# Performance work log

Measured on AMD Instinct MI355X. Metric: run time of the kernel, lower is better.

## Reference

```python
import jax, jax.numpy as jnp
import numpy as np

# dims
N, E, C, HH, HEADS, A, V, D, AE, FH, MAXEL = 10000, 80000, 64, 128, 8, 32, 16, 64, 32, 128, 100
L, K = 2, 9  # lmax=2 -> (L+1)^2 = 9 steerable coefficients
EXPAND = jnp.array([0, 1, 1, 1, 2, 2, 2, 2, 2])          # coeff -> degree l
EXP1 = jnp.array([0, 0, 0, 1, 1, 1, 1, 1])                # coeffs 1..8 -> l-1
L_ONEHOT = jax.nn.one_hot(EXPAND, 3, dtype=jnp.float32)   # [9,3]
COUNTS = jnp.array([1 * C, 3 * C, 5 * C], dtype=jnp.float32)


def so3_linear(h, W, b):
    # per-degree linear (SO3_LinearV2): W [3,Cin,Cout], bias only on l=0
    out = jnp.einsum('nkc,kcd->nkd', h, W[EXPAND])
    return out.at[:, 0].add(b)


def enorm(h):
    # equivariant norm: per-node, per-degree RMS over (m, channels)
    sq = jnp.einsum('nkc,kl->nl', h * h, L_ONEHOT)        # [N,3] sum of squares per l
    scale = jax.lax.rsqrt(sq / COUNTS + 1e-6)             # [N,3]
    return h * scale[:, EXPAND][:, :, None]


def seg_softmax(logits, seg, n):
    m = jax.ops.segment_max(logits, seg, num_segments=n)
    m = jnp.where(jnp.isfinite(m), m, 0.0)
    e = jnp.exp(logits - m[seg])
    s = jax.ops.segment_sum(e, seg, num_segments=n)
    return e / (s[seg] + 1e-9)


def smooth_leaky_relu(z, a=0.2):
    return a * z + (1.0 - a) * z * jax.nn.sigmoid(z)


def setup_inputs():
    key = jax.random.key(0)
    ks = jax.random.split(key, 20)
    p = lambda i, sh, s=0.05: jax.random.normal(ks[i], sh, jnp.float32) * s
    return {
        'x': jax.random.normal(ks[0], (N, K, C), jnp.float32),
        'edge_distance': jax.random.uniform(ks[1], (E, D), dtype=jnp.float32),
        'rl_ij': jax.random.normal(ks[2], (E, K - 1), jnp.float32),
        'src_emb': p(3, (MAXEL, AE), 0.001),
        'tgt_emb': p(4, (MAXEL, AE), 0.001),
        'W1': p(5, (D + 2 * AE, 128)), 'b1': jnp.zeros((128,), jnp.float32),
        'W2': p(6, (128, 3 * 2 * C)), 'b2': jnp.zeros((3 * 2 * C,), jnp.float32),
        'W_conv1': p(7, (3, 2 * C, HH)),
        'W_m0': p(8, (2 * C, HEADS * A + HH + 2 * L * HH)),
        'ln_g': jnp.ones((A,), jnp.float32), 'ln_b': jnp.zeros((A,), jnp.float32),
        'alpha_dot': p(9, (HEADS, A), 0.2),
        'W_xj': p(10, (C, HH)),
        'W_conv2': p(11, (3, HH, HEADS * V)),
        'W_proj': p(12, (3, HEADS * V, C)), 'b_proj': jnp.zeros((C,), jnp.float32),
        'W_gate': p(13, (C, FH)), 'b_gate': jnp.zeros((FH,), jnp.float32),
        'W_ffn1': p(14, (3, C, FH)), 'b_ffn1': jnp.zeros((FH,), jnp.float32),
        'W_ffn2': p(15, (3, FH, C)), 'b_ffn2': jnp.zeros((C,), jnp.float32),
        'atomic_numbers': jax.random.randint(ks[16], (N,), 0, MAXEL),
        'edge_index': jax.random.randint(ks[17], (2, E), 0, N),
    }


def _block(x, edge_distance, rl_ij, src_emb, tgt_emb, W1, b1, W2, b2, W_conv1,
           W_m0, ln_g, ln_b, alpha_dot, W_xj, W_conv2, W_proj, b_proj,
           W_gate, b_gate, W_ffn1, b_ffn1, W_ffn2, b_ffn2,
           atomic_numbers, edge_index):
    src, tgt = edge_index[0], edge_index[1]
    # ---- attention branch (pre-norm) ----
    xn = enorm(x)
    xs, xt = xn[src], xn[tgt]                                    # [E,9,C] gathers
    x_edge = jnp.concatenate([xs, xt], axis=-1)                  # [E,9,2C]
    # radial function with source/target atom embeddings (use_m_share_rad)
    ef = jnp.concatenate([edge_distance, src_emb[atomic_numbers[src]],
                          tgt_emb[atomic_numbers[tgt]]], axis=-1)
    rad = jax.nn.silu(ef @ W1 + b1) @ W2 + b2                    # [E, 3*2C]
    rad = rad.reshape(E, 3, 2 * C)[:, EXPAND]                    # [E,9,2C]
    x_edge = x_edge * rad
    # so2_conv_1: per-degree linear + extra m0 scalar outputs
    msg = jnp.einsum('ekc,kcd->ekd', x_edge, W_conv1[EXPAND])    # [E,9,HH]
    extra = x_edge[:, 0] @ W_m0                                  # [E,896]
    alpha_f = extra[:, :HEADS * A].reshape(E, HEADS, A)
    g_scalar = extra[:, HEADS * A:HEADS * A + HH]                # [E,HH]
    gates = extra[:, HEADS * A + HH:].reshape(E, 2, L, HH)
    g_dir = jax.nn.sigmoid(gates[:, 0])[:, EXP1]                 # [E,8,HH]
    g_ten = jax.nn.sigmoid(gates[:, 1])[:, EXP1]                 # [E,8,HH]
    # GATA value activation: scalar silu + gated direction/tensor terms (l>=1)
    xj_proj = jnp.einsum('ekc,cd->ekd', xs, W_xj)                # [E,9,HH]
    val0 = jax.nn.silu(g_scalar)                                 # [E,HH]
    val_rest = msg[:, 1:] + rl_ij[:, :, None] * g_dir + xj_proj[:, 1:] * g_ten
    val = jnp.concatenate([val0[:, None], val_rest], axis=1)     # [E,9,HH]
    # so2_conv_2
    vout = jnp.einsum('ekd,kdh->ekh', val, W_conv2[EXPAND])      # [E,9,H*V]
    # attention weights
    mu = jnp.mean(alpha_f, axis=-1, keepdims=True)
    var = jnp.var(alpha_f, axis=-1, keepdims=True)
    an = (alpha_f - mu) * jax.lax.rsqrt(var + 1e-5) * ln_g + ln_b
    logits = jnp.einsum('eha,ha->eh', smooth_leaky_relu(an), alpha_dot)
    attn = seg_softmax(logits, tgt, N)                           # [E,HEADS]
    vout = vout.reshape(E, K, HEADS, V) * attn[:, None, :, None]
    node_out = jax.ops.segment_sum(vout.reshape(E, K, HEADS * V), tgt,
                                   num_segments=N)               # [N,9,H*V]
    x = x + so3_linear(node_out, W_proj, b_proj)
    # ---- FFN branch (pre-norm, separable S2-style gating) ----
    yn = enorm(x)
    g = yn[:, 0] @ W_gate + b_gate                               # [N,FH]
    h = so3_linear(yn, W_ffn1, b_ffn1)                           # [N,9,FH]
    h = jnp.concatenate([jax.nn.silu(g)[:, None],
                         h[:, 1:] * jax.nn.sigmoid(g)[:, None, :]], axis=1)
    return x + so3_linear(h, W_ffn2, b_ffn2)


def reference(x, edge_distance, rl_ij, src_emb, tgt_emb, W1, b1, W2, b2,
              W_conv1, W_m0, ln_g, ln_b, alpha_dot, W_xj, W_conv2, W_proj,
              b_proj, W_gate, b_gate, W_ffn1, b_ffn1, W_ffn2, b_ffn2,
              atomic_numbers, edge_index):
    return _block(x, edge_distance, rl_ij, src_emb, tgt_emb, W1, b1, W2, b2,
                  W_conv1, W_m0, ln_g, ln_b, alpha_dot, W_xj, W_conv2, W_proj,
                  b_proj, W_gate, b_gate, W_ffn1, b_ffn1, W_ffn2, b_ffn2,
                  atomic_numbers, edge_index)
```

## Files before the change

kernel.cpp:

```cpp
#include <hip/hip_runtime.h>

#define NN 10000
#define EE 80000

__device__ __forceinline__ float bf2f(unsigned short u) {
  return __uint_as_float(((unsigned)u) << 16);
}
__device__ __forceinline__ unsigned short f2bf(float f) {
  unsigned u = __float_as_uint(f);
  return (unsigned short)((u + 0x7FFFu + ((u >> 16) & 1u)) >> 16);
}
__device__ __forceinline__ float sigm(float x) { return 1.0f / (1.0f + __expf(-x)); }
__device__ __forceinline__ float siluf(float x) { return x * sigm(x); }

__device__ __forceinline__ float ld1(const void* p, long i, bool isf) {
  return isf ? ((const float*)p)[i] : bf2f(((const unsigned short*)p)[i]);
}
__device__ __forceinline__ void st1(void* p, long i, float v, bool isf) {
  if (isf) ((float*)p)[i] = v;
  else     ((unsigned short*)p)[i] = f2bf(v);
}
struct F8 { float v[8]; };
__device__ __forceinline__ F8 ld8(const void* p, long i, bool isf) {
  F8 r;
  if (isf) {
    const float* q = (const float*)p + i;
    float4 a = *(const float4*)q;
    float4 b = *(const float4*)(q + 4);
    r.v[0] = a.x; r.v[1] = a.y; r.v[2] = a.z; r.v[3] = a.w;
    r.v[4] = b.x; r.v[5] = b.y; r.v[6] = b.z; r.v[7] = b.w;
  } else {
    uint4 u = *(const uint4*)((const unsigned short*)p + i);
    r.v[0] = __uint_as_float(u.x << 16); r.v[1] = __uint_as_float(u.x & 0xFFFF0000u);
    r.v[2] = __uint_as_float(u.y << 16); r.v[3] = __uint_as_float(u.y & 0xFFFF0000u);
    r.v[4] = __uint_as_float(u.z << 16); r.v[5] = __uint_as_float(u.z & 0xFFFF0000u);
    r.v[6] = __uint_as_float(u.w << 16); r.v[7] = __uint_as_float(u.w & 0xFFFF0000u);
  }
  return r;
}
__device__ __forceinline__ void ld4v(const void* p, long i, bool isf, float o[4]) {
  if (isf) {
    float4 v = *(const float4*)((const float*)p + i);
    o[0] = v.x; o[1] = v.y; o[2] = v.z; o[3] = v.w;
  } else {
    uint2 u = *(const uint2*)((const unsigned short*)p + i);
    o[0] = bf2f((unsigned short)u.x); o[1] = bf2f((unsigned short)(u.x >> 16));
    o[2] = bf2f((unsigned short)u.y); o[3] = bf2f((unsigned short)(u.y >> 16));
  }
}
__device__ __forceinline__ void ldx4(const unsigned short* p, long i, float o[4]) {
  uint2 u = *(const uint2*)(p + i);
  o[0] = bf2f((unsigned short)u.x); o[1] = bf2f((unsigned short)(u.x >> 16));
  o[2] = bf2f((unsigned short)u.y); o[3] = bf2f((unsigned short)(u.y >> 16));
}
__device__ __forceinline__ void st4bf(unsigned short* dst, float a, float b,
                                      float c, float d) {
  uint2 u;
  u.x = (unsigned)f2bf(a) | ((unsigned)f2bf(b) << 16);
  u.y = (unsigned)f2bf(c) | ((unsigned)f2bf(d) << 16);
  *(uint2*)dst = u;
}
__device__ __forceinline__ float u8f(unsigned v) {
  return (float)(v & 0xFFu) * (1.f / 255.f);
}

typedef __attribute__((ext_vector_type(8))) short bf8v;
typedef __attribute__((ext_vector_type(4))) float f4v;
struct AF128 { bf8v a[4]; };
struct AF64  { bf8v a[2]; };
struct BF128 { bf8v b[4]; };
struct BF64  { bf8v b[2]; };

__device__ __forceinline__ AF128 load_af128(const unsigned short* sA, int pitch, int lane) {
  AF128 f;
  const unsigned short* p = sA + (lane & 15) * pitch + ((lane >> 4) << 3);
#pragma unroll
  for (int kb = 0; kb < 4; ++kb) f.a[kb] = *(const bf8v*)(p + kb * 32);
  return f;
}
__device__ __forceinline__ AF64 load_af64(const unsigned short* sA, int pitch, int lane) {
  AF64 f;
  const unsigned short* p = sA + (lane & 15) * pitch + ((lane >> 4) << 3);
#pragma unroll
  for (int kb = 0; kb < 2; ++kb) f.a[kb] = *(const bf8v*)(p + kb * 32);
  return f;
}
__device__ __forceinline__ BF128 load_b128(const unsigned short* Wt, int row0, int lane) {
  BF128 f;
  const unsigned short* p = Wt + (long)(row0 + (lane & 15)) * 128 + ((lane >> 4) << 3);
#pragma unroll
  for (int kb = 0; kb < 4; ++kb) f.b[kb] = *(const bf8v*)(p + kb * 32);
  return f;
}
__device__ __forceinline__ BF64 load_b64f(const unsigned short* Wt, int row0, int lane) {
  BF64 f;
  const unsigned short* p = Wt + (long)(row0 + (lane & 15)) * 64 + ((lane >> 4) << 3);
#pragma unroll
  for (int kb = 0; kb < 2; ++kb) f.b[kb] = *(const bf8v*)(p + kb * 32);
  return f;
}
__device__ __forceinline__ f4v mfma128f(const AF128& a, const BF128& w) {
  f4v acc = {0.f, 0.f, 0.f, 0.f};
#pragma unroll
  for (int kb = 0; kb < 4; ++kb)
    acc = __builtin_amdgcn_mfma_f32_16x16x32_bf16(a.a[kb], w.b[kb], acc, 0, 0, 0);
  return acc;
}
__device__ __forceinline__ f4v mfma64f(const AF64& a, const BF64& w) {
  f4v acc = {0.f, 0.f, 0.f, 0.f};
#pragma unroll
  for (int kb = 0; kb < 2; ++kb)
    acc = __builtin_amdgcn_mfma_f32_16x16x32_bf16(a.a[kb], w.b[kb], acc, 0, 0, 0);
  return acc;
}
__device__ __forceinline__ f4v mfma128w(const BF128& w, const AF128& x) {
  f4v acc = {0.f, 0.f, 0.f, 0.f};
#pragma unroll
  for (int kb = 0; kb < 4; ++kb)
    acc = __builtin_amdgcn_mfma_f32_16x16x32_bf16(w.b[kb], x.a[kb], acc, 0, 0, 0);
  return acc;
}
__device__ __forceinline__ f4v mfma64w(const BF64& w, const AF64& x) {
  f4v acc = {0.f, 0.f, 0.f, 0.f};
#pragma unroll
  for (int kb = 0; kb < 2; ++kb)
    acc = __builtin_amdgcn_mfma_f32_16x16x32_bf16(w.b[kb], x.a[kb], acc, 0, 0, 0);
  return acc;
}
__device__ __forceinline__ f4v mfma128(const AF128& f, const unsigned short* Wt,
                                       int row0, int lane) {
  return mfma128f(f, load_b128(Wt, row0, lane));
}
__device__ __forceinline__ f4v mfma64(const AF64& f, const unsigned short* Wt,
                                      int row0, int lane) {
  return mfma64f(f, load_b64f(Wt, row0, lane));
}
__device__ __forceinline__ void store8(unsigned short* dst, const unsigned short v[8]) {
  uint4 u;
  u.x = (unsigned)v[0] | ((unsigned)v[1] << 16);
  u.y = (unsigned)v[2] | ((unsigned)v[3] << 16);
  u.z = (unsigned)v[4] | ((unsigned)v[5] << 16);
  u.w = (unsigned)v[6] | ((unsigned)v[7] << 16);
  *(uint4*)dst = u;
}

#define OFF_W1 0
#define OFF_W2 16384
#define OFF_M0 65536
#define OFF_C1 180224
#define OFF_XJ 229376
#define OFF_C2 237568
#define OFF_PJ 286720
#define OFF_G  311296
#define OFF_F1 319488
#define OFF_F2 344064
#define WT_TOTAL 368640

#define WS_SBUF   1177280
#define WS_LOGB   1497280
#define WS_CURS   2777280
#define WS_PERM   2817280
#define WS_NOUT   3137280
#define WS_XN     49217280

__global__ __launch_bounds__(256) void k_repack(
    const void* __restrict__ W1, const void* __restrict__ W2,
    const void* __restrict__ W_m0, const void* __restrict__ W_conv1,
    const void* __restrict__ W_xj, const void* __restrict__ W_conv2,
    const void* __restrict__ W_proj, const void* __restrict__ W_gate,
    const void* __restrict__ W_ffn1, const void* __restrict__ W_ffn2,
    const void* __restrict__ ln_g, unsigned short* __restrict__ wt) {
  const bool isf = (((const unsigned*)ln_g)[0] == 0x3F800000u);
  int i = blockIdx.x * 256 + threadIdx.x;
  float v;
  if (i < 16384)       { int n = i >> 7, k = i & 127; v = ld1(W1, (long)k * 128 + n, isf); }
  else if (i < 65536)  { int j = i - 16384; int n = j >> 7, k = j & 127;
                         v = ld1(W2, (long)k * 384 + n, isf); }
  else if (i < 180224) { int j = i - 65536; int n = j >> 7, k = j & 127;
                         v = ld1(W_m0, (long)k * 896 + n, isf); }
  else if (i < 229376) { int j = i - 180224; int l = j >> 14, r = j & 16383;
                         int n = r >> 7, k = r & 127;
                         v = ld1(W_conv1, (long)(l * 128 + k) * 128 + n, isf); }
  else if (i < 237568) { int j = i - 229376; int n = j >> 6, k = j & 63;
                         v = ld1(W_xj, (long)k * 128 + n, isf); }
  else if (i < 286720) { int j = i - 237568; int l = j >> 14, r = j & 16383;
                         int n = r >> 7, k = r & 127;
                         v = ld1(W_conv2, (long)(l * 128 + k) * 128 + n, isf); }
  else if (i < 311296) { int j = i - 286720; int l = j >> 13, r = j & 8191;
                         int n = r >> 7, k = r & 127;
                         v = ld1(W_proj, (long)(l * 128 + k) * 64 + n, isf); }
  else if (i < 319488) { int j = i - 311296; int n = j >> 6, k = j & 63;
                         v = ld1(W_gate, (long)k * 128 + n, isf); }
  else if (i < 344064) { int j = i - 319488; int l = j >> 13, r = j & 8191;
                         int n = r >> 6, k = r & 63;
                         v = ld1(W_ffn1, (long)(l * 64 + k) * 128 + n, isf); }
  else                 { int j = i - 344064; int l = j >> 13, r = j & 8191;
                         int n = r >> 7, k = r & 127;
                         v = ld1(W_ffn2, (long)(l * 128 + k) * 64 + n, isf); }
  wt[i] = f2bf(v);
}

__global__ __launch_bounds__(256) void k_scales(const void* __restrict__ x,
                                                const void* __restrict__ ln_g,
                                                unsigned short* __restrict__ xn) {
  const bool isf = (((const unsigned*)ln_g)[0] == 0x3F800000u);
  const int n = blockIdx.x * 4 + (threadIdx.x >> 6);
  const int c = threadIdx.x & 63;
  long xb = (long)n * 576;
  float v[9];
#pragma unroll
  for (int k = 0; k < 9; ++k) v[k] = ld1(x, xb + k * 64 + c, isf);
  float q0 = v[0] * v[0], q1 = 0.f, q2 = 0.f;
#pragma unroll
  for (int k = 1; k < 4; ++k) q1 += v[k] * v[k];
#pragma unroll
  for (int k = 4; k < 9; ++k) q2 += v[k] * v[k];
#pragma unroll
  for (int off = 32; off > 0; off >>= 1) {
    q0 += __shfl_xor(q0, off); q1 += __shfl_xor(q1, off); q2 += __shfl_xor(q2, off);
  }
  float s0 = rsqrtf(q0 * (1.f / 64.f)  + 1e-6f);
  float s1 = rsqrtf(q1 * (1.f / 192.f) + 1e-6f);
  float s2 = rsqrtf(q2 * (1.f / 320.f) + 1e-6f);
  xn[xb + c] = f2bf(v[0] * s0);
#pragma unroll
  for (int k = 1; k < 4; ++k) xn[xb + k * 64 + c] = f2bf(v[k] * s1);
#pragma unroll
  for (int k = 4; k < 9; ++k) xn[xb + k * 64 + c] = f2bf(v[k] * s2);
}

__global__ void k_init0(float* __restrict__ p) {
  int i = blockIdx.x * 256 + threadIdx.x;
  if (i < 80000) p[i] = 0.f;
}
__global__ void k_initn(float4* __restrict__ p) {
  int i = blockIdx.x * 256 + threadIdx.x;
  p[i] = make_float4(0.f, 0.f, 0.f, 0.f);
}
__global__ void k_zc(int* __restrict__ c) {
  int i = blockIdx.x * 256 + threadIdx.x;
  if (i < NN) c[i] = 0;
}
__global__ void k_hist(const int* __restrict__ edge_index, int* __restrict__ cnt) {
  int e = blockIdx.x * 256 + threadIdx.x;
  if (e < EE) atomicAdd(&cnt[edge_index[EE + e]], 1);
}
__global__ __launch_bounds__(256) void k_prefix(int* __restrict__ cur) {
  __shared__ int part[256], off0[256];
  const int th = threadIdx.x;
  int cnt[40]; int s = 0;
#pragma unroll 1
  for (int i = 0; i < 40; ++i) {
    int n = th * 40 + i;
    cnt[i] = (n < NN) ? cur[n] : 0;
    s += cnt[i];
  }
  part[th] = s;
  __syncthreads();
  if (th == 0) {
    int acc = 0;
    for (int i = 0; i < 256; ++i) { off0[i] = acc; acc += part[i]; }
  }
  __syncthreads();
  int acc = off0[th];
#pragma unroll 1
  for (int i = 0; i < 40; ++i) {
    int n = th * 40 + i;
    if (n < NN) { cur[n] = acc; acc += cnt[i]; }
  }
}
__global__ void k_scatter(const int* __restrict__ edge_index, int* __restrict__ cur,
                          int* __restrict__ perm) {
  int e = blockIdx.x * 256 + threadIdx.x;
  if (e < EE) {
    int tg = edge_index[EE + e];
    int pos = atomicAdd(&cur[tg], 1);
    perm[pos] = e;
  }
}

__global__ __launch_bounds__(256) void k_logits_e(
    const unsigned short* __restrict__ xn, const void* __restrict__ dist,
    const void* __restrict__ src_emb, const void* __restrict__ tgt_emb,
    const void* __restrict__ b1, const void* __restrict__ b2,
    const void* __restrict__ ln_g, const void* __restrict__ ln_b,
    const void* __restrict__ alpha_dot,
    const int* __restrict__ an, const int* __restrict__ edge_index,
    const unsigned short* __restrict__ wt,
    unsigned short* __restrict__ logitsb, float* __restrict__ sbuf) {
  const bool isf = (((const unsigned*)ln_g)[0] == 0x3F800000u);
  __shared__ int s_src[32], s_tgt[32], s_as[32], s_at[32];
  __shared__ __align__(16) unsigned short sA[32 * 136];
  __shared__ __align__(16) unsigned short sA2[32 * 136];
  __shared__ __align__(16) unsigned short sFB[32 * 264];

  const int t = threadIdx.x;
  const int e0 = blockIdx.x * 32;
  const int lane = t & 63, wave = t >> 6, lm = lane & 15, lq = lane >> 4;

  if (t < 32) {
    int eid = e0 + t;
    int s = edge_index[eid], g = edge_index[EE + eid];
    s_src[t] = s; s_tgt[t] = g;
    s_as[t] = an[s]; s_at[t] = an[g];
  }
  __syncthreads();
#pragma unroll
  for (int ee = 0; ee < 2; ++ee) {
    int e = ee * 16 + (t >> 4), c0 = (t & 15) * 8;
    int eid = e0 + e;
    F8 vv;
    if (c0 < 64)      vv = ld8(dist, (long)eid * 64 + c0, isf);
    else if (c0 < 96) vv = ld8(src_emb, (long)s_as[e] * 32 + (c0 - 64), isf);
    else              vv = ld8(tgt_emb, (long)s_at[e] * 32 + (c0 - 96), isf);
    unsigned short v8[8];
#pragma unroll
    for (int j = 0; j < 8; ++j) v8[j] = f2bf(vv.v[j]);
    store8(&sA[e * 136 + c0], v8);
  }
  __syncthreads();
  {
    AF128 fa0 = load_af128(sA, 136, lane);
    AF128 fa1 = load_af128(sA + 16 * 136, 136, lane);
#pragma unroll
    for (int i = 0; i < 2; ++i) {
      int nt = wave + 4 * i;
      BF128 w = load_b128(wt + OFF_W1, nt * 16, lane);
      f4v d0 = mfma128w(w, fa0);
      f4v d1 = mfma128w(w, fa1);
      int hc = nt * 16 + lq * 4;
      float bb[4]; ld4v(b1, hc, isf, bb);
      st4bf(&sA2[lm * 136 + hc],
            siluf(d0[0] + bb[0]), siluf(d0[1] + bb[1]),
            siluf(d0[2] + bb[2]), siluf(d0[3] + bb[3]));
      st4bf(&sA2[(16 + lm) * 136 + hc],
            siluf(d1[0] + bb[0]), siluf(d1[1] + bb[1]),
            siluf(d1[2] + bb[2]), siluf(d1[3] + bb[3]));
    }
  }
  __syncthreads();
  {
    AF128 fh0 = load_af128(sA2, 136, lane);
    AF128 fh1 = load_af128(sA2 + 16 * 136, 136, lane);
#pragma unroll
    for (int i = 0; i < 2; ++i) {
      int nt = wave + 4 * i;
      BF128 w = load_b128(wt + OFF_W2, nt * 16, lane);
      f4v dd[2] = { mfma128w(w, fh0), mfma128w(w, fh1) };
      int rc = nt * 16 + lq * 4;
      float bb[4]; ld4v(b2, rc, isf, bb);
#pragma unroll
      for (int g = 0; g < 2; ++g) {
        int m = g * 16 + lm;
        float xv[4];
        if (rc < 64) ldx4(xn, (long)s_src[m] * 576 + rc, xv);
        else         ldx4(xn, (long)s_tgt[m] * 576 + (rc - 64), xv);
        st4bf(&sA[m * 136 + rc],
              (dd[g][0] + bb[0]) * xv[0], (dd[g][1] + bb[1]) * xv[1],
              (dd[g][2] + bb[2]) * xv[2], (dd[g][3] + bb[3]) * xv[3]);
      }
    }
  }
  __syncthreads();
  {
    AF128 fe0 = load_af128(sA, 136, lane);
    AF128 fe1 = load_af128(sA + 16 * 136, 136, lane);
#pragma unroll
    for (int i = 0; i < 4; ++i) {
      int nt = wave + 4 * i;
      BF128 w = load_b128(wt + OFF_M0, nt * 16, lane);
      f4v d0 = mfma128w(w, fe0);
      f4v d1 = mfma128w(w, fe1);
      int ac = nt * 16 + lq * 4;
      st4bf(&sFB[lm * 264 + ac], d0[0], d0[1], d0[2], d0[3]);
      st4bf(&sFB[(16 + lm) * 264 + ac], d1[0], d1[1], d1[2], d1[3]);
    }
  }
  __syncthreads();
  {
    int e = t >> 3, h = t & 7;
    const unsigned short* ap = &sFB[e * 264 + h * 32];
    float m1 = 0.f, m2 = 0.f;
#pragma unroll
    for (int a = 0; a < 32; ++a) { float v = bf2f(ap[a]); m1 += v; m2 += v * v; }
    float mu = m1 * (1.f / 32.f);
    float var = m2 * (1.f / 32.f) - mu * mu;
    float rstd = rsqrtf(fmaxf(var, 0.f) + 1e-5f);
    float acc = 0.f;
#pragma unroll
    for (int a = 0; a < 32; ++a) {
      float anv = (bf2f(ap[a]) - mu) * rstd * ld1(ln_g, a, isf) + ld1(ln_b, a, isf);
      float z = 0.2f * anv + 0.8f * anv * sigm(anv);
      acc = fmaf(z, ld1(alpha_dot, (long)h * 32 + a, isf), acc);
    }
    unsigned short lb = f2bf(acc);
    logitsb[(long)(e0 + e) * 8 + h] = lb;
    atomicAdd(&sbuf[s_tgt[e] * 8 + h], __expf(bf2f(lb)));
  }
}

__global__ __launch_bounds__(256, 3) void k_chain_e(
    const unsigned short* __restrict__ xn,
    const void* __restrict__ dist, const void* __restrict__ rl_ij,
    const void* __restrict__ src_emb, const void* __restrict__ tgt_emb,
    const void* __restrict__ b1, const void* __restrict__ b2,
    const void* __restrict__ ln_g,
    const int* __restrict__ an, const int* __restrict__ edge_index,
    const int* __restrict__ perm,
    const unsigned short* __restrict__ wt,
    const unsigned short* __restrict__ logitsb,
    const float* __restrict__ sbuf, float* __restrict__ node_out) {
  const bool isf = (((const unsigned*)ln_g)[0] == 0x3F800000u);
  __shared__ int s_src[16], s_tgt[16], s_as[16], s_at[16], s_eid[16];
  __shared__ float s_aw[16][8], s_rl[16][8];
  __shared__ __align__(16) unsigned short sPOOL[128 * 136];
  __shared__ __align__(16) unsigned short sRAD[16 * 264];
  __shared__ __align__(8) unsigned char sGd[4096];
  __shared__ __align__(8) unsigned char sGt[4096];

  const int t = threadIdx.x;
  const int e0b = blockIdx.x * 16;
  const int lane = t & 63, wave = t >> 6, lm = lane & 15, lq = lane >> 4;

  if (t < 16) {
    int eid = perm[e0b + t];
    int s = edge_index[eid], g = edge_index[EE + eid];
    s_eid[t] = eid;
    s_src[t] = s; s_tgt[t] = g;
    s_as[t] = an[s]; s_at[t] = an[g];
  }
  __syncthreads();

  const int kA = 1 + wave * 2, kB = kA + 1;
  const int lA = (kA < 4) ? 1 : 2, lB = (kB < 4) ? 1 : 2;
  const int gA = lA - 1, gB = lB - 1;
  const long sbase = (long)s_src[lm] * 576 + (lq << 3);
  const long tbase = (long)s_tgt[lm] * 576 + (lq << 3);
  bf8v ggA[4], ggB[4];
  ggA[0] = *(const bf8v*)(xn + sbase + kA * 64);
  ggA[1] = *(const bf8v*)(xn + sbase + kA * 64 + 32);
  ggA[2] = *(const bf8v*)(xn + tbase + kA * 64);
  ggA[3] = *(const bf8v*)(xn + tbase + kA * 64 + 32);
  ggB[0] = *(const bf8v*)(xn + sbase + kB * 64);
  ggB[1] = *(const bf8v*)(xn + sbase + kB * 64 + 32);
  ggB[2] = *(const bf8v*)(xn + tbase + kB * 64);
  ggB[3] = *(const bf8v*)(xn + tbase + kB * 64 + 32);

  if (t < 128) {
    int e = t >> 3, h = t & 7;
    int eid = s_eid[e];
    float ss = sbuf[s_tgt[e] * 8 + h];
    s_aw[e][h] = __expf(bf2f(logitsb[(long)eid * 8 + h])) / (ss + 1e-9f);
    s_rl[e][h] = ld1(rl_ij, (long)eid * 8 + h, isf);
  }
  {
    int e = t >> 4, c0 = (t & 15) * 8;
    int eid = s_eid[e];
    F8 vv;
    if (c0 < 64)      vv = ld8(dist, (long)eid * 64 + c0, isf);
    else if (c0 < 96) vv = ld8(src_emb, (long)s_as[e] * 32 + (c0 - 64), isf);
    else              vv = ld8(tgt_emb, (long)s_at[e] * 32 + (c0 - 96), isf);
    unsigned short v8[8];
#pragma unroll
    for (int j = 0; j < 8; ++j) v8[j] = f2bf(vv.v[j]);
    store8(&sPOOL[e * 136 + c0], v8);
  }
  __syncthreads();
  {
    AF128 fa = load_af128(sPOOL, 136, lane);
#pragma unroll
    for (int i = 0; i < 2; ++i) {
      int nt = wave + 4 * i;
      BF128 w = load_b128(wt + OFF_W1, nt * 16, lane);
      f4v d = mfma128w(w, fa);
      int hc = nt * 16 + lq * 4;
      float bb[4]; ld4v(b1, hc, isf, bb);
      st4bf(&sPOOL[(16 + lm) * 136 + hc],
            siluf(d[0] + bb[0]), siluf(d[1] + bb[1]),
            siluf(d[2] + bb[2]), siluf(d[3] + bb[3]));
    }
  }
  __syncthreads();
  {
    AF128 fh = load_af128(sPOOL + 16 * 136, 136, lane);
#pragma unroll
    for (int i = 0; i < 6; ++i) {
      int nt = wave + 4 * i;
      BF128 w = load_b128(wt + OFF_W2, nt * 16, lane);
      f4v d = mfma128w(w, fh);
      int rc = nt * 16 + lq * 4;
      float bb[4]; ld4v(b2, rc, isf, bb);
      if (i < 2) {
        float xv[4];
        if (rc < 64) ldx4(xn, (long)s_src[lm] * 576 + rc, xv);
        else         ldx4(xn, (long)s_tgt[lm] * 576 + (rc - 64), xv);
        st4bf(&sPOOL[lm * 136 + rc],
              (d[0] + bb[0]) * xv[0], (d[1] + bb[1]) * xv[1],
              (d[2] + bb[2]) * xv[2], (d[3] + bb[3]) * xv[3]);
      } else {
        st4bf(&sRAD[lm * 264 + (rc - 128)],
              d[0] + bb[0], d[1] + bb[1], d[2] + bb[2], d[3] + bb[3]);
      }
    }
  }
  __syncthreads();
  {
    AF128 fe = load_af128(sPOOL, 136, lane);
#pragma unroll
    for (int i = 0; i < 10; ++i) {
      int nt = wave + 4 * i;
      BF128 w = load_b128(wt + OFF_M0 + 256 * 128, nt * 16, lane);
      f4v d = mfma128w(w, fe);
      int oc = nt * 16 + lq * 4;
      if (i < 2) {
        st4bf(&sPOOL[(16 + lm) * 136 + oc],
              siluf(d[0]), siluf(d[1]), siluf(d[2]), siluf(d[3]));
      } else {
        int c = oc - 128;
        unsigned q0 = __float2uint_rn(sigm(d[0]) * 255.f);
        unsigned q1 = __float2uint_rn(sigm(d[1]) * 255.f);
        unsigned q2 = __float2uint_rn(sigm(d[2]) * 255.f);
        unsigned q3 = __float2uint_rn(sigm(d[3]) * 255.f);
        unsigned pk = q0 | (q1 << 8) | (q2 << 16) | (q3 << 24);
        if (c < 256) *(unsigned*)&sGd[lm * 256 + c]         = pk;
        else         *(unsigned*)&sGt[lm * 256 + (c - 256)] = pk;
      }
    }
  }
  __syncthreads();
  {
    AF128 fv = load_af128(sPOOL + 16 * 136, 136, lane);
#pragma unroll
    for (int i = 0; i < 2; ++i) {
      int nt = wave + 4 * i;
      f4v d = mfma128(fv, wt + OFF_C2, nt * 16, lane);
      int col = nt * 16 + lm, h = col >> 4;
      float acc = 0.f; int cur = s_tgt[lq * 4];
#pragma unroll
      for (int r = 0; r < 4; ++r) {
        int m = lq * 4 + r;
        int tg = s_tgt[m];
        float v = s_aw[m][h] * d[r];
        if (tg != cur) {
          atomicAdd(&node_out[(long)cur * 1152 + col], acc);
          acc = 0.f; cur = tg;
        }
        acc += v;
      }
      atomicAdd(&node_out[(long)cur * 1152 + col], acc);
    }
  }
  __syncthreads();

  {
    const int er = lm;
    const float rlA = s_rl[er][kA - 1], rlB = s_rl[er][kB - 1];
    AF128 fmA, fmB; AF64 fxA, fxB;
    fxA.a[0] = ggA[0]; fxA.a[1] = ggA[1];
    fxB.a[0] = ggB[0]; fxB.a[1] = ggB[1];
    const unsigned short* rpA = sRAD + er * 264 + gA * 128 + (lq << 3);
    const unsigned short* rpB = sRAD + er * 264 + gB * 128 + (lq << 3);
#pragma unroll
    for (int kb = 0; kb < 4; ++kb) {
      bf8v rvA = *(const bf8v*)(rpA + kb * 32);
      bf8v rvB = *(const bf8v*)(rpB + kb * 32);
      bf8v oA, oB;
#pragma unroll
      for (int j = 0; j < 8; ++j) {
        oA[j] = (short)f2bf(bf2f((unsigned short)ggA[kb][j]) *
                            bf2f((unsigned short)rvA[j]));
        oB[j] = (short)f2bf(bf2f((unsigned short)ggB[kb][j]) *
                            bf2f((unsigned short)rvB[j]));
      }
      fmA.a[kb] = oA; fmB.a[kb] = oB;
    }
    unsigned short* vbA = sPOOL + (wave * 32) * 136;
    unsigned short* vbB = vbA + 16 * 136;
#pragma unroll
    for (int mt = 0; mt < 8; ++mt) {
      BF128 w1A = load_b128(wt + OFF_C1 + lA * 16384, mt * 16, lane);
      BF128 w1B;
      if (lB == lA) w1B = w1A;
      else          w1B = load_b128(wt + OFF_C1 + lB * 16384, mt * 16, lane);
      BF64 wx = load_b64f(wt + OFF_XJ, mt * 16, lane);
      f4v dmA = mfma128w(w1A, fmA);
      f4v dmB = mfma128w(w1B, fmB);
      f4v dxA = mfma64w(wx, fxA);
      f4v dxB = mfma64w(wx, fxB);
      int d0 = mt * 16 + lq * 4;
      unsigned gdA = *(const unsigned*)&sGd[er * 256 + (gA << 7) + d0];
      unsigned gtA = *(const unsigned*)&sGt[er * 256 + (gA << 7) + d0];
      unsigned gdB, gtB;
      if (gB == gA) { gdB = gdA; gtB = gtA; }
      else {
        gdB = *(const unsigned*)&sGd[er * 256 + (gB << 7) + d0];
        gtB = *(const unsigned*)&sGt[er * 256 + (gB << 7) + d0];
      }
      st4bf(&vbA[er * 136 + d0],
            dmA[0] + rlA * u8f(gdA)       + dxA[0] * u8f(gtA),
            dmA[1] + rlA * u8f(gdA >> 8)  + dxA[1] * u8f(gtA >> 8),
            dmA[2] + rlA * u8f(gdA >> 16) + dxA[2] * u8f(gtA >> 16),
            dmA[3] + rlA * u8f(gdA >> 24) + dxA[3] * u8f(gtA >> 24));
      st4bf(&vbB[er * 136 + d0],
            dmB[0] + rlB * u8f(gdB)       + dxB[0] * u8f(gtB),
            dmB[1] + rlB * u8f(gdB >> 8)  + dxB[1] * u8f(gtB >> 8),
            dmB[2] + rlB * u8f(gdB >> 16) + dxB[2] * u8f(gtB >> 16),
            dmB[3] + rlB * u8f(gdB >> 24) + dxB[3] * u8f(gtB >> 24));
    }
    AF128 fvA = load_af128(vbA, 136, lane);
    AF128 fvB = load_af128(vbB, 136, lane);
#pragma unroll
    for (int nt = 0; nt < 8; ++nt) {
      const int col = nt * 16 + lm;
      BF128 w2A = load_b128(wt + OFF_C2 + lA * 16384, nt * 16, lane);
      BF128 w2B;
      if (lB == lA) w2B = w2A;
      else          w2B = load_b128(wt + OFF_C2 + lB * 16384, nt * 16, lane);
      f4v dA = mfma128f(fvA, w2A);
      f4v dB = mfma128f(fvB, w2B);
      float accA = 0.f, accB = 0.f; int cur = s_tgt[lq * 4];
#pragma unroll
      for (int r = 0; r < 4; ++r) {
        int m = lq * 4 + r;
        int tg = s_tgt[m];
        if (tg != cur) {
          atomicAdd(&node_out[(long)cur * 1152 + kA * 128 + col], accA);
          atomicAdd(&node_out[(long)cur * 1152 + kB * 128 + col], accB);
          accA = 0.f; accB = 0.f; cur = tg;
        }
        accA += s_aw[m][nt] * dA[r];
        accB += s_aw[m][nt] * dB[r];
      }
      atomicAdd(&node_out[(long)cur * 1152 + kA * 128 + col], accA);
      atomicAdd(&node_out[(long)cur * 1152 + kB * 128 + col], accB);
    }
  }
}

__global__ __launch_bounds__(256) void k_epi_mfma(
    const void* __restrict__ x,
    const void* __restrict__ b_proj, const void* __restrict__ b_gate,
    const void* __restrict__ b_ffn2, const void* __restrict__ ln_g,
    const unsigned short* __restrict__ wt,
    const float* __restrict__ node_out, void* __restrict__ out) {
  const bool isf = (((const unsigned*)ln_g)[0] == 0x3F800000u);
  __shared__ __align__(16) char POOL[96768];
  unsigned short* sIN = (unsigned short*)POOL;
  float* sXN = (float*)(POOL + 39168);
  unsigned short* sYN = (unsigned short*)(POOL + 76032);
  unsigned short* sH  = sIN;
  __shared__ float s_sgf[16][128];
  __shared__ float s_nsc[16][3];

  const int t = threadIdx.x;
  const int n0 = blockIdx.x * 16;
  const int lane = t & 63, wave = t >> 6, lm = lane & 15, lq = lane >> 4;

#pragma unroll
  for (int it = 0; it < 9; ++it) {
    int u = t + it * 256;
    int row = u >> 4, c0 = (u & 15) * 8;
    int k = row >> 4, n = row & 15;
    const float4* q = (const float4*)&node_out[(long)(n0 + n) * 1152 + k * 128 + c0];
    float4 a = q[0], b = q[1];
    unsigned short v8[8] = { f2bf(a.x), f2bf(a.y), f2bf(a.z), f2bf(a.w),
                             f2bf(b.x), f2bf(b.y), f2bf(b.z), f2bf(b.w) };
    store8(&sIN[row * 136 + c0], v8);
  }
  __syncthreads();
  for (int tid = wave; tid < 36; tid += 4) {
    int mt = tid >> 2, ntile = tid & 3;
    int l = (mt == 0) ? 0 : ((mt < 4) ? 1 : 2);
    AF128 fa = load_af128(sIN + mt * 16 * 136, 136, lane);
    f4v d = mfma128(fa, wt + OFF_PJ + l * 8192, ntile * 16, lane);
    int col = ntile * 16 + lm;
#pragma unroll
    for (int r = 0; r < 4; ++r) {
      int row = mt * 16 + lq * 4 + r;
      int n = row & 15, k = mt;
      float v = d[r] + ld1(x, (long)(n0 + n) * 576 + k * 64 + col, isf);
      if (k == 0) v += ld1(b_proj, col, isf);
      sXN[row * 64 + col] = v;
    }
  }
  __syncthreads();
  {
    int n = t >> 4, c4 = (t & 15) * 4;
    float q0 = 0.f, q1 = 0.f, q2 = 0.f;
#pragma unroll
    for (int k = 0; k < 9; ++k)
#pragma unroll
      for (int j = 0; j < 4; ++j) {
        float v = sXN[(k * 16 + n) * 64 + c4 + j];
        float vv = v * v;
        if (k == 0) q0 += vv; else if (k < 4) q1 += vv; else q2 += vv;
      }
#pragma unroll
    for (int off = 8; off > 0; off >>= 1) {
      q0 += __shfl_xor(q0, off); q1 += __shfl_xor(q1, off); q2 += __shfl_xor(q2, off);
    }
    if ((t & 15) == 0) {
      s_nsc[n][0] = rsqrtf(q0 * (1.f / 64.f)  + 1e-6f);
      s_nsc[n][1] = rsqrtf(q1 * (1.f / 192.f) + 1e-6f);
      s_nsc[n][2] = rsqrtf(q2 * (1.f / 320.f) + 1e-6f);
    }
  }
  __syncthreads();
#pragma unroll
  for (int it = 0; it < 5; ++it) {
    int u = t + it * 256;
    if (u < 1152) {
      int row = u >> 3, c0 = (u & 7) * 8;
      int k = row >> 4, n = row & 15;
      int l = (k == 0) ? 0 : ((k < 4) ? 1 : 2);
      float sc = s_nsc[n][l];
      unsigned short v8[8];
#pragma unroll
      for (int j = 0; j < 8; ++j) v8[j] = f2bf(sXN[row * 64 + c0 + j] * sc);
      store8(&sYN[row * 72 + c0], v8);
    }
  }
  __syncthreads();
  {
    AF64 fg = load_af64(sYN, 72, lane);
    for (int nt = wave; nt < 8; nt += 4) {
      f4v d = mfma64(fg, wt + OFF_G, nt * 16, lane);
      int col = nt * 16 + lm;
#pragma unroll
      for (int r = 0; r < 4; ++r) {
        int n = lq * 4 + r;
        float gv = d[r] + ld1(b_gate, col, isf);
        float sg = sigm(gv);
        s_sgf[n][col] = sg;
        sH[n * 136 + col] = f2bf(gv * sg);
      }
    }
  }
  __syncthreads();
  for (int tid = wave; tid < 64; tid += 4) {
    int mt = 1 + (tid >> 3), ntile = tid & 7;
    int l = (mt < 4) ? 1 : 2;
    AF64 fy = load_af64(sYN + mt * 16 * 72, 72, lane);
    f4v d = mfma64(fy, wt + OFF_F1 + l * 8192, ntile * 16, lane);
    int col = ntile * 16 + lm;
#pragma unroll
    for (int r = 0; r < 4; ++r) {
      int row = mt * 16 + lq * 4 + r;
      int n = row & 15;
      sH[row * 136 + col] = f2bf(d[r] * s_sgf[n][col]);
    }
  }
  __syncthreads();
  for (int tid = wave; tid < 36; tid += 4) {
    int mt = tid >> 2, ntile = tid & 3;
    int l = (mt == 0) ? 0 : ((mt < 4) ? 1 : 2);
    AF128 fh = load_af128(sH + mt * 16 * 136, 136, lane);
    f4v d = mfma128(fh, wt + OFF_F2 + l * 8192, ntile * 16, lane);
    int col = ntile * 16 + lm;
#pragma unroll
    for (int r = 0; r < 4; ++r) {
      int row = mt * 16 + lq * 4 + r;
      int n = row & 15, k = mt;
      float v = sXN[row * 64 + col] + d[r];
      if (k == 0) v += ld1(b_ffn2, col, isf);
      st1(out, (long)(n0 + n) * 576 + k * 64 + col, v, isf);
    }
  }
}

extern "C" void kernel_launch(void* const* d_in, const int* in_sizes, int n_in,
                              void* d_out, int out_size, void* d_ws, size_t ws_size,
                              hipStream_t stream) {
  (void)in_sizes; (void)n_in; (void)out_size; (void)ws_size;
  char* ws = (char*)d_ws;
  unsigned short* wt   = (unsigned short*)ws;
  float*    sbuf       = (float*)(ws + WS_SBUF);
  unsigned short* logb = (unsigned short*)(ws + WS_LOGB);
  int*      cursor     = (int*)(ws + WS_CURS);
  int*      perm       = (int*)(ws + WS_PERM);
  float*    node_out   = (float*)(ws + WS_NOUT);
  unsigned short* xnb  = (unsigned short*)(ws + WS_XN);
  const int* an        = (const int*)d_in[24];
  const int* ei        = (const int*)d_in[25];

  k_repack<<<WT_TOTAL / 256, 256, 0, stream>>>(
      d_in[5], d_in[7], d_in[10], d_in[9], d_in[14], d_in[15],
      d_in[16], d_in[18], d_in[20], d_in[22], d_in[11], wt);
  k_scales<<<NN / 4, 256, 0, stream>>>(d_in[0], d_in[11], xnb);
  k_init0<<<313, 256, 0, stream>>>(sbuf);
  k_initn<<<11250, 256, 0, stream>>>((float4*)node_out);
  k_zc<<<40, 256, 0, stream>>>(cursor);
  k_hist<<<(EE + 255) / 256, 256, 0, stream>>>(ei, cursor);
  k_prefix<<<1, 256, 0, stream>>>(cursor);
  k_scatter<<<(EE + 255) / 256, 256, 0, stream>>>(ei, cursor, perm);
  k_logits_e<<<EE / 32, 256, 0, stream>>>(
      xnb, d_in[1], d_in[3], d_in[4], d_in[6], d_in[8],
      d_in[11], d_in[12], d_in[13], an, ei, wt, logb, sbuf);
  k_chain_e<<<EE / 16, 256, 0, stream>>>(
      xnb, d_in[1], d_in[2], d_in[3], d_in[4], d_in[6], d_in[8], d_in[11],
      an, ei, perm, wt, logb, sbuf, node_out);
  k_epi_mfma<<<NN / 16, 256, 0, stream>>>(
      d_in[0], d_in[17], d_in[19], d_in[23], d_in[11], wt, node_out, d_out);
}
```

Before: 847.3 us.

## Process 32 edges per block in k_chain_e to reuse weight fragments

The edge chain kernel now handles two 16-edge M-tiles per block, so each weight B-fragment loaded for the W1, W2, M0 and conv MFMAs is used twice. This halves the number of blocks and the weight-load traffic per edge. Gate byte buffers are padded to a 264-byte row stride, and launch bounds drop from 3 to 2 to leave room for the extra registers. The risk is lower occupancy and more register pressure, and the second tile's gathers being serialized after the first.

```diff
diff --git a/kernel.cpp b/kernel.cpp
--- a/kernel.cpp
+++ b/kernel.cpp
@@ -399,7 +399,7 @@
   }
 }
 
-__global__ __launch_bounds__(256, 3) void k_chain_e(
+__global__ __launch_bounds__(256, 2) void k_chain_e(
     const unsigned short* __restrict__ xn,
     const void* __restrict__ dist, const void* __restrict__ rl_ij,
     const void* __restrict__ src_emb, const void* __restrict__ tgt_emb,
@@ -411,18 +411,18 @@
     const unsigned short* __restrict__ logitsb,
     const float* __restrict__ sbuf, float* __restrict__ node_out) {
   const bool isf = (((const unsigned*)ln_g)[0] == 0x3F800000u);
-  __shared__ int s_src[16], s_tgt[16], s_as[16], s_at[16], s_eid[16];
-  __shared__ float s_aw[16][8], s_rl[16][8];
+  __shared__ int s_src[32], s_tgt[32], s_as[32], s_at[32], s_eid[32];
+  __shared__ float s_aw[32][8], s_rl[32][8];
   __shared__ __align__(16) unsigned short sPOOL[128 * 136];
-  __shared__ __align__(16) unsigned short sRAD[16 * 264];
-  __shared__ __align__(8) unsigned char sGd[4096];
-  __shared__ __align__(8) unsigned char sGt[4096];
+  __shared__ __align__(16) unsigned short sRAD[32 * 264];
+  __shared__ __align__(8) unsigned char sGd[32 * 264];
+  __shared__ __align__(8) unsigned char sGt[32 * 264];
 
   const int t = threadIdx.x;
-  const int e0b = blockIdx.x * 16;
+  const int e0b = blockIdx.x * 32;
   const int lane = t & 63, wave = t >> 6, lm = lane & 15, lq = lane >> 4;
 
-  if (t < 16) {
+  if (t < 32) {
     int eid = perm[e0b + t];
     int s = edge_index[eid], g = edge_index[EE + eid];
     s_eid[t] = eid;
@@ -434,27 +434,31 @@
   const int kA = 1 + wave * 2, kB = kA + 1;
   const int lA = (kA < 4) ? 1 : 2, lB = (kB < 4) ? 1 : 2;
   const int gA = lA - 1, gB = lB - 1;
-  const long sbase = (long)s_src[lm] * 576 + (lq << 3);
-  const long tbase = (long)s_tgt[lm] * 576 + (lq << 3);
-  bf8v ggA[4], ggB[4];
-  ggA[0] = *(const bf8v*)(xn + sbase + kA * 64);
-  ggA[1] = *(const bf8v*)(xn + sbase + kA * 64 + 32);
-  ggA[2] = *(const bf8v*)(xn + tbase + kA * 64);
-  ggA[3] = *(const bf8v*)(xn + tbase + kA * 64 + 32);
-  ggB[0] = *(const bf8v*)(xn + sbase + kB * 64);
-  ggB[1] = *(const bf8v*)(xn + sbase + kB * 64 + 32);
-  ggB[2] = *(const bf8v*)(xn + tbase + kB * 64);
-  ggB[3] = *(const bf8v*)(xn + tbase + kB * 64 + 32);
-
-  if (t < 128) {
+  bf8v gg[2][2][4];
+  {
+    const long sb0 = (long)s_src[lm] * 576 + (lq << 3);
+    const long tb0 = (long)s_tgt[lm] * 576 + (lq << 3);
+    gg[0][0][0] = *(const bf8v*)(xn + sb0 + kA * 64);
+    gg[0][0][1] = *(const bf8v*)(xn + sb0 + kA * 64 + 32);
+    gg[0][0][2] = *(const bf8v*)(xn + tb0 + kA * 64);
+    gg[0][0][3] = *(const bf8v*)(xn + tb0 + kA * 64 + 32);
+    gg[0][1][0] = *(const bf8v*)(xn + sb0 + kB * 64);
+    gg[0][1][1] = *(const bf8v*)(xn + sb0 + kB * 64 + 32);
+    gg[0][1][2] = *(const bf8v*)(xn + tb0 + kB * 64);
+    gg[0][1][3] = *(const bf8v*)(xn + tb0 + kB * 64 + 32);
+  }
+
+  {
     int e = t >> 3, h = t & 7;
     int eid = s_eid[e];
     float ss = sbuf[s_tgt[e] * 8 + h];
     s_aw[e][h] = __expf(bf2f(logitsb[(long)eid * 8 + h])) / (ss + 1e-9f);
     s_rl[e][h] = ld1(rl_ij, (long)eid * 8 + h, isf);
   }
-  {
-    int e = t >> 4, c0 = (t & 15) * 8;
+#pragma unroll
+  for (int it = 0; it < 2; ++it) {
+    int u = t + it * 256;
+    int e = u >> 4, c0 = (u & 15) * 8;
     int eid = s_eid[e];
     F8 vv;
     if (c0 < 64)      vv = ld8(dist, (long)eid * 64 + c0, isf);
@@ -467,172 +471,217 @@
   }
   __syncthreads();
   {
-    AF128 fa = load_af128(sPOOL, 136, lane);
+    AF128 fa0 = load_af128(sPOOL, 136, lane);
+    AF128 fa1 = load_af128(sPOOL + 16 * 136, 136, lane);
 #pragma unroll
     for (int i = 0; i < 2; ++i) {
       int nt = wave + 4 * i;
       BF128 w = load_b128(wt + OFF_W1, nt * 16, lane);
-      f4v d = mfma128w(w, fa);
+      f4v d0 = mfma128w(w, fa0);
+      f4v d1 = mfma128w(w, fa1);
       int hc = nt * 16 + lq * 4;
       float bb[4]; ld4v(b1, hc, isf, bb);
-      st4bf(&sPOOL[(16 + lm) * 136 + hc],
-            siluf(d[0] + bb[0]), siluf(d[1] + bb[1]),
-            siluf(d[2] + bb[2]), siluf(d[3] + bb[3]));
-    }
-  }
-  __syncthreads();
-  {
-    AF128 fh = load_af128(sPOOL + 16 * 136, 136, lane);
+      st4bf(&sPOOL[(32 + lm) * 136 + hc],
+            siluf(d0[0] + bb[0]), siluf(d0[1] + bb[1]),
+            siluf(d0[2] + bb[2]), siluf(d0[3] + bb[3]));
+      st4bf(&sPOOL[(48 + lm) * 136 + hc],
+            siluf(d1[0] + bb[0]), siluf(d1[1] + bb[1]),
+            siluf(d1[2] + bb[2]), siluf(d1[3] + bb[3]));
+    }
+  }
+  __syncthreads();
+  {
+    AF128 fh0 = load_af128(sPOOL + 32 * 136, 136, lane);
+    AF128 fh1 = load_af128(sPOOL + 48 * 136, 136, lane);
 #pragma unroll
     for (int i = 0; i < 6; ++i) {
       int nt = wave + 4 * i;
       BF128 w = load_b128(wt + OFF_W2, nt * 16, lane);
-      f4v d = mfma128w(w, fh);
+      f4v dd[2] = { mfma128w(w, fh0), mfma128w(w, fh1) };
       int rc = nt * 16 + lq * 4;
       float bb[4]; ld4v(b2, rc, isf, bb);
       if (i < 2) {
-        float xv[4];
-        if (rc < 64) ldx4(xn, (long)s_src[lm] * 576 + rc, xv);
-        else         ldx4(xn, (long)s_tgt[lm] * 576 + (rc - 64), xv);
-        st4bf(&sPOOL[lm * 136 + rc],
-              (d[0] + bb[0]) * xv[0], (d[1] + bb[1]) * xv[1],
-              (d[2] + bb[2]) * xv[2], (d[3] + bb[3]) * xv[3]);
+#pragma unroll
+        for (int g = 0; g < 2; ++g) {
+          int m = g * 16 + lm;
+          float xv[4];
+          if (rc < 64) ldx4(xn, (long)s_src[m] * 576 + rc, xv);
+          else         ldx4(xn, (long)s_tgt[m] * 576 + (rc - 64), xv);
+          st4bf(&sPOOL[m * 136 + rc],
+                (dd[g][0] + bb[0]) * xv[0], (dd[g][1] + bb[1]) * xv[1],
+                (dd[g][2] + bb[2]) * xv[2], (dd[g][3] + bb[3]) * xv[3]);
+        }
       } else {
         st4bf(&sRAD[lm * 264 + (rc - 128)],
-              d[0] + bb[0], d[1] + bb[1], d[2] + bb[2], d[3] + bb[3]);
+              dd[0][0] + bb[0], dd[0][1] + bb[1],
+              dd[0][2] + bb[2], dd[0][3] + bb[3]);
+        st4bf(&sRAD[(16 + lm) * 264 + (rc - 128)],
+              dd[1][0] + bb[0], dd[1][1] + bb[1],
+              dd[1][2] + bb[2], dd[1][3] + bb[3]);
       }
     }
   }
   __syncthreads();
   {
-    AF128 fe = load_af128(sPOOL, 136, lane);
+    AF128 fe0 = load_af128(sPOOL, 136, lane);
+    AF128 fe1 = load_af128(sPOOL + 16 * 136, 136, lane);
 #pragma unroll
     for (int i = 0; i < 10; ++i) {
       int nt = wave + 4 * i;
       BF128 w = load_b128(wt + OFF_M0 + 256 * 128, nt * 16, lane);
-      f4v d = mfma128w(w, fe);
+      f4v d0 = mfma128w(w, fe0);
+      f4v d1 = mfma128w(w, fe1);
       int oc = nt * 16 + lq * 4;
       if (i < 2) {
-        st4bf(&sPOOL[(16 + lm) * 136 + oc],
-              siluf(d[0]), siluf(d[1]), siluf(d[2]), siluf(d[3]));
+        st4bf(&sPOOL[(32 + lm) * 136 + oc],
+              siluf(d0[0]), siluf(d0[1]), siluf(d0[2]), siluf(d0[3]));
+        st4bf(&sPOOL[(48 + lm) * 136 + oc],
+              siluf(d1[0]), siluf(d1[1]), siluf(d1[2]), siluf(d1[3]));
       } else {
         int c = oc - 128;
-        unsigned q0 = __float2uint_rn(sigm(d[0]) * 255.f);
-        unsigned q1 = __float2uint_rn(sigm(d[1]) * 255.f);
-        unsigned q2 = __float2uint_rn(sigm(d[2]) * 255.f);
-        unsigned q3 = __float2uint_rn(sigm(d[3]) * 255.f);
-        unsigned pk = q0 | (q1 << 8) | (q2 << 16) | (q3 << 24);
-        if (c < 256) *(unsigned*)&sGd[lm * 256 + c]         = pk;
-        else         *(unsigned*)&sGt[lm * 256 + (c - 256)] = pk;
+#pragma unroll
+        for (int g = 0; g < 2; ++g) {
+          f4v d = g ? d1 : d0;
+          int row = g * 16 + lm;
+          unsigned q0 = __float2uint_rn(sigm(d[0]) * 255.f);
+          unsigned q1 = __float2uint_rn(sigm(d[1]) * 255.f);
+          unsigned q2 = __float2uint_rn(sigm(d[2]) * 255.f);
+          unsigned q3 = __float2uint_rn(sigm(d[3]) * 255.f);
+          unsigned pk = q0 | (q1 << 8) | (q2 << 16) | (q3 << 24);
+          if (c < 256) *(unsigned*)&sGd[row * 264 + c]         = pk;
+          else         *(unsigned*)&sGt[row * 264 + (c - 256)] = pk;
+        }
       }
     }
   }
   __syncthreads();
   {
-    AF128 fv = load_af128(sPOOL + 16 * 136, 136, lane);
+    AF128 fv0 = load_af128(sPOOL + 32 * 136, 136, lane);
+    AF128 fv1 = load_af128(sPOOL + 48 * 136, 136, lane);
 #pragma unroll
     for (int i = 0; i < 2; ++i) {
       int nt = wave + 4 * i;
-      f4v d = mfma128(fv, wt + OFF_C2, nt * 16, lane);
-      int col = nt * 16 + lm, h = col >> 4;
-      float acc = 0.f; int cur = s_tgt[lq * 4];
-#pragma unroll
-      for (int r = 0; r < 4; ++r) {
-        int m = lq * 4 + r;
-        int tg = s_tgt[m];
-        float v = s_aw[m][h] * d[r];
-        if (tg != cur) {
-          atomicAdd(&node_out[(long)cur * 1152 + col], acc);
-          acc = 0.f; cur = tg;
+      BF128 w2 = load_b128(wt + OFF_C2, nt * 16, lane);
+      f4v d0 = mfma128f(fv0, w2);
+      f4v d1 = mfma128f(fv1, w2);
+      int col = nt * 16 + lm;
+#pragma unroll
+      for (int g = 0; g < 2; ++g) {
+        f4v d = g ? d1 : d0;
+        float acc = 0.f; int cur = s_tgt[g * 16 + lq * 4];
+#pragma unroll
+        for (int r = 0; r < 4; ++r) {
+          int m = g * 16 + lq * 4 + r;
+          int tg = s_tgt[m];
+          float v = s_aw[m][nt] * d[r];
+          if (tg != cur) {
+            atomicAdd(&node_out[(long)cur * 1152 + col], acc);
+            acc = 0.f; cur = tg;
+          }
+          acc += v;
         }
-        acc += v;
+        atomicAdd(&node_out[(long)cur * 1152 + col], acc);
       }
-      atomicAdd(&node_out[(long)cur * 1152 + col], acc);
-    }
-  }
-  __syncthreads();
-
-  {
-    const int er = lm;
-    const float rlA = s_rl[er][kA - 1], rlB = s_rl[er][kB - 1];
-    AF128 fmA, fmB; AF64 fxA, fxB;
-    fxA.a[0] = ggA[0]; fxA.a[1] = ggA[1];
-    fxB.a[0] = ggB[0]; fxB.a[1] = ggB[1];
-    const unsigned short* rpA = sRAD + er * 264 + gA * 128 + (lq << 3);
-    const unsigned short* rpB = sRAD + er * 264 + gB * 128 + (lq << 3);
-#pragma unroll
-    for (int kb = 0; kb < 4; ++kb) {
-      bf8v rvA = *(const bf8v*)(rpA + kb * 32);
-      bf8v rvB = *(const bf8v*)(rpB + kb * 32);
-      bf8v oA, oB;
-#pragma unroll
-      for (int j = 0; j < 8; ++j) {
-        oA[j] = (short)f2bf(bf2f((unsigned short)ggA[kb][j]) *
-                            bf2f((unsigned short)rvA[j]));
-        oB[j] = (short)f2bf(bf2f((unsigned short)ggB[kb][j]) *
-                            bf2f((unsigned short)rvB[j]));
-      }
-      fmA.a[kb] = oA; fmB.a[kb] = oB;
+    }
+  }
+  __syncthreads();
+
+  {
+    {
+      const long sb1 = (long)s_src[16 + lm] * 576 + (lq << 3);
+      const long tb1 = (long)s_tgt[16 + lm] * 576 + (lq << 3);
+      gg[1][0][0] = *(const bf8v*)(xn + sb1 + kA * 64);
+      gg[1][0][1] = *(const bf8v*)(xn + sb1 + kA * 64 + 32);
+      gg[1][0][2] = *(const bf8v*)(xn + tb1 + kA * 64);
+      gg[1][0][3] = *(const bf8v*)(xn + tb1 + kA * 64 + 32);
+      gg[1][1][0] = *(const bf8v*)(xn + sb1 + kB * 64);
+      gg[1][1][1] = *(const bf8v*)(xn + sb1 + kB * 64 + 32);
+      gg[1][1][2] = *(const bf8v*)(xn + tb1 + kB * 64);
+      gg[1][1][3] = *(const bf8v*)(xn + tb1 + kB * 64 + 32);
     }
     unsigned short* vbA = sPOOL + (wave * 32) * 136;
     unsigned short* vbB = vbA + 16 * 136;
 #pragma unroll
-    for (int mt = 0; mt < 8; ++mt) {
-      BF128 w1A = load_b128(wt + OFF_C1 + lA * 16384, mt * 16, lane);
-      BF128 w1B;
-      if (lB == lA) w1B = w1A;
-      else          w1B = load_b128(wt + OFF_C1 + lB * 16384, mt * 16, lane);
-      BF64 wx = load_b64f(wt + OFF_XJ, mt * 16, lane);
-      f4v dmA = mfma128w(w1A, fmA);
-      f4v dmB = mfma128w(w1B, fmB);
-      f4v dxA = mfma64w(wx, fxA);
-      f4v dxB = mfma64w(wx, fxB);
-      int d0 = mt * 16 + lq * 4;
-      unsigned gdA = *(const unsigned*)&sGd[er * 256 + (gA << 7) + d0];
-      unsigned gtA = *(const unsigned*)&sGt[er * 256 + (gA << 7) + d0];
-      unsigned gdB, gtB;
-      if (gB == gA) { gdB = gdA; gtB = gtA; }
-      else {
-        gdB = *(const unsigned*)&sGd[er * 256 + (gB << 7) + d0];
-        gtB = *(const unsigned*)&sGt[er * 256 + (gB << 7) + d0];
+    for (int g = 0; g < 2; ++g) {
+      const int er = g * 16 + lm;
+      const float rlA = s_rl[er][kA - 1], rlB = s_rl[er][kB - 1];
+      AF128 fmA, fmB; AF64 fxA, fxB;
+      fxA.a[0] = gg[g][0][0]; fxA.a[1] = gg[g][0][1];
+      fxB.a[0] = gg[g][1][0]; fxB.a[1] = gg[g][1][1];
+      const unsigned short* rpA = sRAD + er * 264 + gA * 128 + (lq << 3);
+      const unsigned short* rpB = sRAD + er * 264 + gB * 128 + (lq << 3);
+#pragma unroll
+      for (int kb = 0; kb < 4; ++kb) {
+        bf8v rvA = *(const bf8v*)(rpA + kb * 32);
+        bf8v rvB = *(const bf8v*)(rpB + kb * 32);
+        bf8v oA, oB;
+#pragma unroll
+        for (int j = 0; j < 8; ++j) {
+          oA[j] = (short)f2bf(bf2f((unsigned short)gg[g][0][kb][j]) *
+                              bf2f((unsigned short)rvA[j]));
+          oB[j] = (short)f2bf(bf2f((unsigned short)gg[g][1][kb][j]) *
+                              bf2f((unsigned short)rvB[j]));
+        }
+        fmA.a[kb] = oA; fmB.a[kb] = oB;
       }
-      st4bf(&vbA[er * 136 + d0],
-            dmA[0] + rlA * u8f(gdA)       + dxA[0] * u8f(gtA),
-            dmA[1] + rlA * u8f(gdA >> 8)  + dxA[1] * u8f(gtA >> 8),
-            dmA[2] + rlA * u8f(gdA >> 16) + dxA[2] * u8f(gtA >> 16),
-            dmA[3] + rlA * u8f(gdA >> 24) + dxA[3] * u8f(gtA >> 24));
-      st4bf(&vbB[er * 136 + d0],
-            dmB[0] + rlB * u8f(gdB)       + dxB[0] * u8f(gtB),
-            dmB[1] + rlB * u8f(gdB >> 8)  + dxB[1] * u8f(gtB >> 8),
-            dmB[2] + rlB * u8f(gdB >> 16) + dxB[2] * u8f(gtB >> 16),
-            dmB[3] + rlB * u8f(gdB >> 24) + dxB[3] * u8f(gtB >> 24));
-    }
-    AF128 fvA = load_af128(vbA, 136, lane);
-    AF128 fvB = load_af128(vbB, 136, lane);
-#pragma unroll
-    for (int nt = 0; nt < 8; ++nt) {
-      const int col = nt * 16 + lm;
-      BF128 w2A = load_b128(wt + OFF_C2 + lA * 16384, nt * 16, lane);
-      BF128 w2B;
-      if (lB == lA) w2B = w2A;
-      else          w2B = load_b128(wt + OFF_C2 + lB * 16384, nt * 16, lane);
-      f4v dA = mfma128f(fvA, w2A);
-      f4v dB = mfma128f(fvB, w2B);
-      float accA = 0.f, accB = 0.f; int cur = s_tgt[lq * 4];
-#pragma unroll
-      for (int r = 0; r < 4; ++r) {
-        int m = lq * 4 + r;
-        int tg = s_tgt[m];
-        if (tg != cur) {
-          atomicAdd(&node_out[(long)cur * 1152 + kA * 128 + col], accA);
-          atomicAdd(&node_out[(long)cur * 1152 + kB * 128 + col], accB);
-          accA = 0.f; accB = 0.f; cur = tg;
+#pragma unroll
+      for (int mt = 0; mt < 8; ++mt) {
+        BF128 w1A = load_b128(wt + OFF_C1 + lA * 16384, mt * 16, lane);
+        BF128 w1B;
+        if (lB == lA) w1B = w1A;
+        else          w1B = load_b128(wt + OFF_C1 + lB * 16384, mt * 16, lane);
+        BF64 wx = load_b64f(wt + OFF_XJ, mt * 16, lane);
+        f4v dmA = mfma128w(w1A, fmA);
+        f4v dmB = mfma128w(w1B, fmB);
+        f4v dxA = mfma64w(wx, fxA);
+        f4v dxB = mfma64w(wx, fxB);
+        int d0 = mt * 16 + lq * 4;
+        unsigned gdA = *(const unsigned*)&sGd[er * 264 + (gA << 7) + d0];
+        unsigned gtA = *(const unsigned*)&sGt[er * 264 + (gA << 7) + d0];
+        unsigned gdB, gtB;
+        if (gB == gA) { gdB = gdA; gtB = gtA; }
+        else {
+          gdB = *(const unsigned*)&sGd[er * 264 + (gB << 7) + d0];
+          gtB = *(const unsigned*)&sGt[er * 264 + (gB << 7) + d0];
         }
-        accA += s_aw[m][nt] * dA[r];
-        accB += s_aw[m][nt] * dB[r];
+        st4bf(&vbA[lm * 136 + d0],
+              dmA[0] + rlA * u8f(gdA)       + dxA[0] * u8f(gtA),
+              dmA[1] + rlA * u8f(gdA >> 8)  + dxA[1] * u8f(gtA >> 8),
+              dmA[2] + rlA * u8f(gdA >> 16) + dxA[2] * u8f(gtA >> 16),
+              dmA[3] + rlA * u8f(gdA >> 24) + dxA[3] * u8f(gtA >> 24));
+        st4bf(&vbB[lm * 136 + d0],
+              dmB[0] + rlB * u8f(gdB)       + dxB[0] * u8f(gtB),
+              dmB[1] + rlB * u8f(gdB >> 8)  + dxB[1] * u8f(gtB >> 8),
+              dmB[2] + rlB * u8f(gdB >> 16) + dxB[2] * u8f(gtB >> 16),
+              dmB[3] + rlB * u8f(gdB >> 24) + dxB[3] * u8f(gtB >> 24));
       }
-      atomicAdd(&node_out[(long)cur * 1152 + kA * 128 + col], accA);
-      atomicAdd(&node_out[(long)cur * 1152 + kB * 128 + col], accB);
+      AF128 fvA = load_af128(vbA, 136, lane);
+      AF128 fvB = load_af128(vbB, 136, lane);
+#pragma unroll
+      for (int nt = 0; nt < 8; ++nt) {
+        const int col = nt * 16 + lm;
+        BF128 w2A = load_b128(wt + OFF_C2 + lA * 16384, nt * 16, lane);
+        BF128 w2B;
+        if (lB == lA) w2B = w2A;
+        else          w2B = load_b128(wt + OFF_C2 + lB * 16384, nt * 16, lane);
+        f4v dA = mfma128f(fvA, w2A);
+        f4v dB = mfma128f(fvB, w2B);
+        float accA = 0.f, accB = 0.f; int cur = s_tgt[g * 16 + lq * 4];
+#pragma unroll
+        for (int r = 0; r < 4; ++r) {
+          int m = g * 16 + lq * 4 + r;
+          int tg = s_tgt[m];
+          if (tg != cur) {
+            atomicAdd(&node_out[(long)cur * 1152 + kA * 128 + col], accA);
+            atomicAdd(&node_out[(long)cur * 1152 + kB * 128 + col], accB);
+            accA = 0.f; accB = 0.f; cur = tg;
+          }
+          accA += s_aw[m][nt] * dA[r];
+          accB += s_aw[m][nt] * dB[r];
+        }
+        atomicAdd(&node_out[(long)cur * 1152 + kA * 128 + col], accA);
+        atomicAdd(&node_out[(long)cur * 1152 + kB * 128 + col], accB);
+      }
     }
   }
 }
@@ -796,7 +845,7 @@
   k_logits_e<<<EE / 32, 256, 0, stream>>>(
       xnb, d_in[1], d_in[3], d_in[4], d_in[6], d_in[8],
       d_in[11], d_in[12], d_in[13], an, ei, wt, logb, sbuf);
-  k_chain_e<<<EE / 16, 256, 0, stream>>>(
+  k_chain_e<<<EE / 32, 256, 0, stream>>>(
       xnb, d_in[1], d_in[2], d_in[3], d_in[4], d_in[6], d_in[8], d_in[11],
       an, ei, perm, wt, logb, sbuf, node_out);
   k_epi_mfma<<<NN / 16, 256, 0, stream>>>(
```

Measured after the change: 776.0 us. 1.09x faster.
